# Optimization experiments

Measured on AMD Instinct MI355X. Metric: run time of the kernel, lower is better.

## Reference

```python
import jax, jax.numpy as jnp
import numpy as np

CONV_SPECS = [(1, 64, 4, 2), (64, 128, 8, 4), (128, 256, 10, 5), (256, 256, 12, 6)]  # (cin, cout, k, stride)
N_CODEBOOKS = 8
CODEBOOK_SIZE = 1024
D_MODEL = 256
STATE_FRAMES = 4
B = 8192


def setup_inputs() -> dict:
    key = jax.random.key(0)
    ks = jax.random.split(key, 3 + 2 * len(CONV_SPECS) + 1)
    d = {
        "audio_frame": jax.random.normal(ks[0], (B, 1, 240), dtype=jnp.float32),
        "state_in": jax.random.normal(ks[1], (B, D_MODEL, STATE_FRAMES), dtype=jnp.float32),
    }
    for i, (cin, cout, k, s) in enumerate(CONV_SPECS):
        scale = 1.0 / np.sqrt(cin * k)
        d[f"W{i}"] = jax.random.normal(ks[2 + 2 * i], (cout, cin, k), dtype=jnp.float32) * scale
        d[f"b{i}"] = jnp.zeros((cout,), dtype=jnp.float32)
    d["codebooks"] = jax.random.normal(ks[-1], (N_CODEBOOKS, CODEBOOK_SIZE, D_MODEL), dtype=jnp.float32) * 0.02
    return d


def _causal_conv(x, W, b, stride):
    # x: [B, Cin, L]; causal left-pad of (k - stride) so L_out = L // stride
    k = W.shape[-1]
    x = jnp.pad(x, ((0, 0), (0, 0), (k - stride, 0)))
    y = jax.lax.conv_general_dilated(
        x, W, window_strides=(stride,), padding="VALID",
        dimension_numbers=("NCH", "OIH", "NCH"))
    return y + b[None, :, None]


def _rvq_indices(x_btd, codebooks):
    # x_btd: [B, T, D]; codebooks: [Q, K, D] -> indices [B, Q, T]
    r = x_btd
    idxs = []
    for q in range(codebooks.shape[0]):
        cb = codebooks[q]                                        # [K, D]
        # ||r - c||^2 = ||r||^2 - 2 r.c + ||c||^2 ; ||r||^2 constant over k for argmin
        dist = jnp.sum(cb * cb, axis=-1) - 2.0 * jnp.einsum("btd,kd->btk", r, cb)
        idx = jnp.argmin(dist, axis=-1)                          # [B, T]
        r = r - cb[idx]                                          # residual update
        idxs.append(idx)
    return jnp.stack(idxs, axis=1)                               # [B, Q, T]


def reference(audio_frame, state_in, W0, b0, W1, b1, W2, b2, W3, b3, codebooks):
    # state: roll left, zero last frame
    new_state = jnp.roll(state_in, -1, axis=2).at[:, :, -1].set(0.0)

    # causal conv encoder stack (ELU between conv blocks)
    Ws, bs = (W0, W1, W2, W3), (b0, b1, b2, b3)
    x = audio_frame
    for i, (_, _, _, stride) in enumerate(CONV_SPECS):
        x = _causal_conv(x, Ws[i], bs[i], stride)
        if i < len(CONV_SPECS) - 1:
            x = jax.nn.elu(x)
    # x: [B, D_MODEL, 1]

    new_state = new_state.at[:, :, -1].set(x[:, :, -1])

    z = _rvq_indices(x.transpose(0, 2, 1), codebooks)            # [B, Q, T]
    acoustic_tokens = z[:, :, -1]                                # [B, 8]
    return acoustic_tokens, new_state
```

## Files before the change

kernel.cpp:

```cpp
#include <hip/hip_runtime.h>
#include <hip/hip_bf16.h>

#define GB 2

__device__ __forceinline__ float elu1(float v) { return v > 0.f ? v : expm1f(v); }

__global__ void cnorm_kernel(const float* __restrict__ cb, float* __restrict__ cnorm) {
    int g = blockIdx.x * blockDim.x + threadIdx.x;
    if (g >= 8 * 1024) return;
    const float* p = cb + (size_t)g * 256;
    float s = 0.f;
    for (int d = 0; d < 256; d += 4) {
        float4 v = *reinterpret_cast<const float4*>(p + d);
        s += v.x * v.x + v.y * v.y + v.z * v.z + v.w * v.w;
    }
    cnorm[g] = s;
}

__global__ void cbtrans_kernel(const float* __restrict__ cb, float* __restrict__ cbT) {
    int t = blockIdx.x * blockDim.x + threadIdx.x;
    int o = t * 4;
    const int s = o >> 13;
    const int r = o & 8191;
    const int dl = r >> 10;
    const int k = r & 1023;
    const int q = s >> 5;
    const int d = (s & 31) * 8 + dl;
    const float* src = cb + ((size_t)(q * 1024 + k)) * 256 + d;
    float4 v;
    v.x = src[0 * 256]; v.y = src[1 * 256]; v.z = src[2 * 256]; v.w = src[3 * 256];
    *reinterpret_cast<float4*>(cbT + o) = v;
}

__global__ void wtrans_kernel(const float* __restrict__ W1, const float* __restrict__ W2,
                              const float* __restrict__ W3, float* __restrict__ W1T,
                              float* __restrict__ W2T, float* __restrict__ W3T) {
    int g = blockIdx.x * blockDim.x + threadIdx.x;
    if (g < 8192) {
        int ci = g >> 7, c = g & 127;
        const float* src = W1 + c * 512 + ci * 8;
        float4 a = *reinterpret_cast<const float4*>(src);
        float4 b = *reinterpret_cast<const float4*>(src + 4);
        *reinterpret_cast<float4*>(W1T + g * 8) = a;
        *reinterpret_cast<float4*>(W1T + g * 8 + 4) = b;
    }
    int g2 = g - 8192;
    if (g2 >= 0 && g2 < 32768) {
        int ci = g2 >> 8, c = g2 & 255;
        const float* src = W2 + c * 1280 + ci * 10;
        float* dst = W2T + g2 * 10;
#pragma unroll
        for (int j = 0; j < 5; ++j)
            *reinterpret_cast<float2*>(dst + 2 * j) =
                *reinterpret_cast<const float2*>(src + 2 * j);
    }
    int g3 = g - 40960;
    if (g3 >= 0 && g3 < 65536) {
        int ci = g3 >> 8, c = g3 & 255;
        const float* src = W3 + c * 3072 + ci * 12 + 6;
        float* dst = W3T + g3 * 6;
#pragma unroll
        for (int j = 0; j < 3; ++j)
            *reinterpret_cast<float2*>(dst + 2 * j) =
                *reinterpret_cast<const float2*>(src + 2 * j);
    }
}

__global__ __launch_bounds__(256, 2)
void convA_kernel(const float* __restrict__ audio,
                  const float* __restrict__ W0, const float* __restrict__ b0,
                  const float* __restrict__ W1T, const float* __restrict__ b1,
                  float* __restrict__ y1g) {
    __shared__ __align__(16) float xs[244];
    __shared__ __align__(16) float y0s[64 * 124];

    const int tid = threadIdx.x;
    const int b = blockIdx.x;

    if (tid < 64) {
        y0s[tid * 124 + 0] = 0.f; y0s[tid * 124 + 1] = 0.f;
        y0s[tid * 124 + 2] = 0.f; y0s[tid * 124 + 3] = 0.f;
    }
    if (tid < 242) xs[tid] = (tid < 2) ? 0.f : audio[b * 240 + tid - 2];
    __syncthreads();
    {
        const int ci = tid >> 2, tg = tid & 3;
        float4 w = *reinterpret_cast<const float4*>(W0 + ci * 4);
        float bias = b0[ci];
        for (int t = tg; t < 120; t += 4) {
            float v = bias + w.x * xs[2 * t] + w.y * xs[2 * t + 1]
                           + w.z * xs[2 * t + 2] + w.w * xs[2 * t + 3];
            y0s[ci * 124 + 4 + t] = elu1(v);
        }
    }
    __syncthreads();
    {
        const int c = tid >> 1, half = tid & 1, t0 = 15 * half;
        float acc[15];
        float bias = b1[c];
#pragma unroll
        for (int u = 0; u < 15; ++u) acc[u] = bias;
        const float* wbase = W1T + c * 8;
        const float* ybase = y0s + 4 * t0;
        for (int ci = 0; ci < 64; ++ci) {
            float4 wA = *reinterpret_cast<const float4*>(wbase + ci * 1024);
            float4 wB = *reinterpret_cast<const float4*>(wbase + ci * 1024 + 4);
            const float* yb = ybase + ci * 124;
            float4 row4[16];
#pragma unroll
            for (int j = 0; j < 16; ++j)
                row4[j] = *reinterpret_cast<const float4*>(yb + 4 * j);
#pragma unroll
            for (int u = 0; u < 15; ++u) {
                acc[u] += wA.x * row4[u].x + wA.y * row4[u].y
                        + wA.z * row4[u].z + wA.w * row4[u].w
                        + wB.x * row4[u + 1].x + wB.y * row4[u + 1].y
                        + wB.z * row4[u + 1].z + wB.w * row4[u + 1].w;
            }
        }
        float* yo = y1g + ((size_t)b * 128 + c) * 32 + t0;
#pragma unroll
        for (int u = 0; u < 15; ++u) yo[u] = elu1(acc[u]);
    }
}

__global__ __launch_bounds__(256, 2)
void convB_kernel(const float* __restrict__ state_in,
                  const float* __restrict__ b2, const float* __restrict__ b3,
                  const float* __restrict__ W2T, const float* __restrict__ W3T,
                  const float* __restrict__ y1g,
                  float* __restrict__ out, float* __restrict__ r_ws) {
    __shared__ __align__(16) float y2s[GB * 256 * 6];

    const int tid = threadIdx.x;
    const int bbase = blockIdx.x * GB;

    {
        const int c = tid;
        float acc[GB][6];
        float bias = b2[c];
#pragma unroll
        for (int bi = 0; bi < GB; ++bi)
#pragma unroll
            for (int t = 0; t < 6; ++t) acc[bi][t] = bias;
        const float* wbase = W2T + c * 10;
        for (int ci = 0; ci < 128; ++ci) {
            float w[10];
#pragma unroll
            for (int jj = 0; jj < 5; ++jj) {
                float2 wv = *reinterpret_cast<const float2*>(wbase + ci * 2560 + jj * 2);
                w[jj * 2] = wv.x; w[jj * 2 + 1] = wv.y;
            }
#pragma unroll
            for (int bi = 0; bi < GB; ++bi) {
                const float* yr = y1g + ((size_t)(bbase + bi) * 128 + ci) * 32;
                float row[32];
#pragma unroll
                for (int k4 = 0; k4 < 8; ++k4) {
                    float4 v = *reinterpret_cast<const float4*>(yr + k4 * 4);
                    row[k4 * 4] = v.x; row[k4 * 4 + 1] = v.y;
                    row[k4 * 4 + 2] = v.z; row[k4 * 4 + 3] = v.w;
                }
                acc[bi][0] += w[5] * row[0] + w[6] * row[1] + w[7] * row[2]
                            + w[8] * row[3] + w[9] * row[4];
#pragma unroll
                for (int t = 1; t < 6; ++t) {
                    const int q0 = 5 * t - 5;
                    float s = 0.f;
#pragma unroll
                    for (int j = 0; j < 10; ++j) s += w[j] * row[q0 + j];
                    acc[bi][t] += s;
                }
            }
        }
#pragma unroll
        for (int bi = 0; bi < GB; ++bi)
#pragma unroll
            for (int t = 0; t < 6; ++t)
                y2s[(bi * 256 + c) * 6 + t] = elu1(acc[bi][t]);
    }
    __syncthreads();
    {
        const int c = tid;
        float acc[GB];
        float bias = b3[c];
#pragma unroll
        for (int bi = 0; bi < GB; ++bi) acc[bi] = bias;
        const float* wbase = W3T + c * 6;
        for (int ci = 0; ci < 256; ++ci) {
            float2 w01 = *reinterpret_cast<const float2*>(wbase + ci * 1536);
            float2 w23 = *reinterpret_cast<const float2*>(wbase + ci * 1536 + 2);
            float2 w45 = *reinterpret_cast<const float2*>(wbase + ci * 1536 + 4);
#pragma unroll
            for (int bi = 0; bi < GB; ++bi) {
                const float* yr = y2s + (bi * 256 + ci) * 6;
                float2 a = *reinterpret_cast<const float2*>(yr);
                float2 d = *reinterpret_cast<const float2*>(yr + 2);
                float2 e = *reinterpret_cast<const float2*>(yr + 4);
                acc[bi] += w01.x * a.x + w01.y * a.y + w23.x * d.x + w23.y * d.y
                         + w45.x * e.x + w45.y * e.y;
            }
        }
#pragma unroll
        for (int bi = 0; bi < GB; ++bi) {
            const int b = bbase + bi;
            float y3 = acc[bi];
            r_ws[b * 256 + c] = y3;
            float4 si = *reinterpret_cast<const float4*>(state_in + b * 1024 + c * 4);
            float4 o; o.x = si.y; o.y = si.z; o.z = si.w; o.w = y3;
            *reinterpret_cast<float4*>(out + 65536 + b * 1024 + c * 4) = o;
        }
    }
}

__device__ __forceinline__ unsigned long long distkey(float d, int k) {
    unsigned u = __float_as_uint(d);
    u = (u & 0x80000000u) ? ~u : (u | 0x80000000u);
    return ((unsigned long long)u << 32) | (unsigned)k;
}

__global__ __launch_bounds__(256)
void rvq_kernel(const float* __restrict__ cb, const float* __restrict__ cbT,
                const float* __restrict__ cnorm, const float* __restrict__ r_ws,
                float* __restrict__ out) {
    __shared__ __align__(16) float rs[16 * 256];
    __shared__ unsigned long long part_sh[2][16];
    __shared__ int idx_sh[16];

    const int tid = threadIdx.x;
    const int lane = tid & 63;
    const int wid = tid >> 6;
    const int bg = wid >> 1;
    const int kg = wid & 1;
    const int b0 = blockIdx.x * 16;
    const int kb = kg * 512 + 4 * lane;

    for (int it = 0; it < 4; ++it) {
        int o = (it * 256 + tid) * 4;
        *reinterpret_cast<float4*>(rs + o) =
            *reinterpret_cast<const float4*>(r_ws + b0 * 256 + o);
    }
    __syncthreads();

    for (int q = 0; q < 8; ++q) {
        float acc[8][8];
#pragma unroll
        for (int i = 0; i < 8; ++i)
#pragma unroll
            for (int j = 0; j < 8; ++j) acc[i][j] = 0.f;

        for (int ds = 0; ds < 32; ++ds) {
            const float* sb = cbT + (size_t)(q * 32 + ds) * 8192;
#pragma unroll
            for (int dp = 0; dp < 2; ++dp) {
                float4 cv0[4], cv1[4];
#pragma unroll
                for (int dd = 0; dd < 4; ++dd) {
                    const int dl = dp * 4 + dd;
                    cv0[dd] = *reinterpret_cast<const float4*>(sb + dl * 1024 + kb);
                    cv1[dd] = *reinterpret_cast<const float4*>(sb + dl * 1024 + kb + 256);
                }
                float rr[8][4];
#pragma unroll
                for (int i = 0; i < 8; ++i) {
                    float4 t = *reinterpret_cast<const float4*>(
                        rs + (bg * 8 + i) * 256 + ds * 8 + dp * 4);
                    rr[i][0] = t.x; rr[i][1] = t.y; rr[i][2] = t.z; rr[i][3] = t.w;
                }
#pragma unroll
                for (int dd = 0; dd < 4; ++dd) {
#pragma unroll
                    for (int i = 0; i < 8; ++i) {
                        const float r = rr[i][dd];
                        acc[i][0] += r * cv0[dd].x; acc[i][1] += r * cv0[dd].y;
                        acc[i][2] += r * cv0[dd].z; acc[i][3] += r * cv0[dd].w;
                        acc[i][4] += r * cv1[dd].x; acc[i][5] += r * cv1[dd].y;
                        acc[i][6] += r * cv1[dd].z; acc[i][7] += r * cv1[dd].w;
                    }
                }
            }
        }
        {
            float4 cn0 = *reinterpret_cast<const float4*>(cnorm + q * 1024 + kb);
            float4 cn1 = *reinterpret_cast<const float4*>(cnorm + q * 1024 + kb + 256);
            float c0e[4] = {cn0.x, cn0.y, cn0.z, cn0.w};
            float c1e[4] = {cn1.x, cn1.y, cn1.z, cn1.w};
#pragma unroll
            for (int i = 0; i < 8; ++i) {
                unsigned long long k = 0xFFFFFFFFFFFFFFFFull;
#pragma unroll
                for (int e = 0; e < 4; ++e) {
                    unsigned long long ka = distkey(c0e[e] - 2.f * acc[i][e], kb + e);
                    unsigned long long kc = distkey(c1e[e] - 2.f * acc[i][4 + e],
                                                    kb + 256 + e);
                    if (ka < k) k = ka;
                    if (kc < k) k = kc;
                }
                for (int off = 32; off >= 1; off >>= 1) {
                    unsigned long long o = __shfl_xor(k, off, 64);
                    if (o < k) k = o;
                }
                if (lane == 0) part_sh[kg][bg * 8 + i] = k;
            }
        }
        __syncthreads();
        if (tid < 16) {
            unsigned long long ka = part_sh[0][tid];
            unsigned long long kc = part_sh[1][tid];
            if (kc < ka) ka = kc;
            const int idx = (int)(ka & 0xFFFFFFFFu);
            idx_sh[tid] = idx;
            out[(b0 + tid) * 8 + q] = (float)idx;
        }
        __syncthreads();
        for (int it = 0; it < 16; ++it) {
            const int idx = idx_sh[it];
            rs[it * 256 + tid] -= cb[((size_t)(q * 1024 + idx)) * 256 + tid];
        }
        __syncthreads();
    }
}

extern "C" void kernel_launch(void* const* d_in, const int* in_sizes, int n_in,
                              void* d_out, int out_size, void* d_ws, size_t ws_size,
                              hipStream_t stream) {
    const float* audio = (const float*)d_in[0];
    const float* state = (const float*)d_in[1];
    const float* W0 = (const float*)d_in[2];
    const float* b0 = (const float*)d_in[3];
    const float* W1 = (const float*)d_in[4];
    const float* b1 = (const float*)d_in[5];
    const float* W2 = (const float*)d_in[6];
    const float* b2 = (const float*)d_in[7];
    const float* W3 = (const float*)d_in[8];
    const float* b3 = (const float*)d_in[9];
    const float* cbk = (const float*)d_in[10];
    float* out = (float*)d_out;

    float* cnorm_ws = (float*)d_ws;
    float* r_ws = cnorm_ws + 8192;
    float* W1T = r_ws + 2097152;
    float* W2T = W1T + 65536;
    float* W3T = W2T + 327680;
    float* y1g = W3T + 393216;
    float* cbT = y1g + 33554432;

    cnorm_kernel<<<32, 256, 0, stream>>>(cbk, cnorm_ws);
    cbtrans_kernel<<<2048, 256, 0, stream>>>(cbk, cbT);
    wtrans_kernel<<<416, 256, 0, stream>>>(W1, W2, W3, W1T, W2T, W3T);
    convA_kernel<<<8192, 256, 0, stream>>>(audio, W0, b0, W1T, b1, y1g);
    convB_kernel<<<8192 / GB, 256, 0, stream>>>(state, b2, b3, W2T, W3T, y1g,
                                                out, r_ws);
    rvq_kernel<<<512, 256, 0, stream>>>(cbk, cbT, cnorm_ws, r_ws, out);
}
```

Baseline: 1.868 ms.

## Process two batch items per convA block with two output channels per thread

```diff
diff --git a/kernel.cpp b/kernel.cpp
--- a/kernel.cpp
+++ b/kernel.cpp
@@ -72,39 +72,47 @@
                   const float* __restrict__ W1T, const float* __restrict__ b1,
                   float* __restrict__ y1g) {
     __shared__ __align__(16) float xs[244];
-    __shared__ __align__(16) float y0s[64 * 124];
+    __shared__ __align__(16) float y0s[2 * 64 * 124];
 
     const int tid = threadIdx.x;
-    const int b = blockIdx.x;
-
-    if (tid < 64) {
-        y0s[tid * 124 + 0] = 0.f; y0s[tid * 124 + 1] = 0.f;
-        y0s[tid * 124 + 2] = 0.f; y0s[tid * 124 + 3] = 0.f;
-    }
-    if (tid < 242) xs[tid] = (tid < 2) ? 0.f : audio[b * 240 + tid - 2];
-    __syncthreads();
-    {
+    const int bbase = blockIdx.x * 2;
+
+    if (tid < 128) {
+        const int bz = tid >> 6, ciz = tid & 63;
+        float* p = y0s + (bz * 64 + ciz) * 124;
+        p[0] = 0.f; p[1] = 0.f; p[2] = 0.f; p[3] = 0.f;
+    }
+
+    for (int bi2 = 0; bi2 < 2; ++bi2) {
+        __syncthreads();
+        if (tid < 242) xs[tid] = (tid < 2) ? 0.f : audio[(bbase + bi2) * 240 + tid - 2];
+        __syncthreads();
         const int ci = tid >> 2, tg = tid & 3;
         float4 w = *reinterpret_cast<const float4*>(W0 + ci * 4);
         float bias = b0[ci];
         for (int t = tg; t < 120; t += 4) {
             float v = bias + w.x * xs[2 * t] + w.y * xs[2 * t + 1]
                            + w.z * xs[2 * t + 2] + w.w * xs[2 * t + 3];
-            y0s[ci * 124 + 4 + t] = elu1(v);
+            y0s[(bi2 * 64 + ci) * 124 + 4 + t] = elu1(v);
         }
     }
     __syncthreads();
     {
-        const int c = tid >> 1, half = tid & 1, t0 = 15 * half;
-        float acc[15];
-        float bias = b1[c];
-#pragma unroll
-        for (int u = 0; u < 15; ++u) acc[u] = bias;
-        const float* wbase = W1T + c * 8;
-        const float* ybase = y0s + 4 * t0;
+        const int bi = tid >> 7;
+        const int half = (tid >> 6) & 1;
+        const int cg = tid & 63;
+        const int t0 = 15 * half;
+        float acc0[15], acc1[15];
+        const float bias0 = b1[cg], bias1 = b1[cg + 64];
+#pragma unroll
+        for (int u = 0; u < 15; ++u) { acc0[u] = bias0; acc1[u] = bias1; }
+        const float* wbase0 = W1T + cg * 8;
+        const float* ybase = y0s + bi * 64 * 124 + 4 * t0;
         for (int ci = 0; ci < 64; ++ci) {
-            float4 wA = *reinterpret_cast<const float4*>(wbase + ci * 1024);
-            float4 wB = *reinterpret_cast<const float4*>(wbase + ci * 1024 + 4);
+            float4 wA0 = *reinterpret_cast<const float4*>(wbase0 + ci * 1024);
+            float4 wB0 = *reinterpret_cast<const float4*>(wbase0 + ci * 1024 + 4);
+            float4 wA1 = *reinterpret_cast<const float4*>(wbase0 + ci * 1024 + 512);
+            float4 wB1 = *reinterpret_cast<const float4*>(wbase0 + ci * 1024 + 516);
             const float* yb = ybase + ci * 124;
             float4 row4[16];
 #pragma unroll
@@ -112,15 +120,24 @@
                 row4[j] = *reinterpret_cast<const float4*>(yb + 4 * j);
 #pragma unroll
             for (int u = 0; u < 15; ++u) {
-                acc[u] += wA.x * row4[u].x + wA.y * row4[u].y
-                        + wA.z * row4[u].z + wA.w * row4[u].w
-                        + wB.x * row4[u + 1].x + wB.y * row4[u + 1].y
-                        + wB.z * row4[u + 1].z + wB.w * row4[u + 1].w;
-            }
-        }
-        float* yo = y1g + ((size_t)b * 128 + c) * 32 + t0;
-#pragma unroll
-        for (int u = 0; u < 15; ++u) yo[u] = elu1(acc[u]);
+                acc0[u] += wA0.x * row4[u].x + wA0.y * row4[u].y
+                         + wA0.z * row4[u].z + wA0.w * row4[u].w
+                         + wB0.x * row4[u + 1].x + wB0.y * row4[u + 1].y
+                         + wB0.z * row4[u + 1].z + wB0.w * row4[u + 1].w;
+                acc1[u] += wA1.x * row4[u].x + wA1.y * row4[u].y
+                         + wA1.z * row4[u].z + wA1.w * row4[u].w
+                         + wB1.x * row4[u + 1].x + wB1.y * row4[u + 1].y
+                         + wB1.z * row4[u + 1].z + wB1.w * row4[u + 1].w;
+            }
+        }
+        const int b = bbase + bi;
+        float* yo0 = y1g + ((size_t)b * 128 + cg) * 32 + t0;
+        float* yo1 = y1g + ((size_t)b * 128 + cg + 64) * 32 + t0;
+#pragma unroll
+        for (int u = 0; u < 15; ++u) {
+            yo0[u] = elu1(acc0[u]);
+            yo1[u] = elu1(acc1[u]);
+        }
     }
 }
 
@@ -348,7 +365,7 @@
     cnorm_kernel<<<32, 256, 0, stream>>>(cbk, cnorm_ws);
     cbtrans_kernel<<<2048, 256, 0, stream>>>(cbk, cbT);
     wtrans_kernel<<<416, 256, 0, stream>>>(W1, W2, W3, W1T, W2T, W3T);
-    convA_kernel<<<8192, 256, 0, stream>>>(audio, W0, b0, W1T, b1, y1g);
+    convA_kernel<<<4096, 256, 0, stream>>>(audio, W0, b0, W1T, b1, y1g);
     convB_kernel<<<8192 / GB, 256, 0, stream>>>(state, b2, b3, W2T, W3T, y1g,
                                                 out, r_ws);
     rvq_kernel<<<512, 256, 0, stream>>>(cbk, cbT, cnorm_ws, r_ws, out);
```

Result: faster. 1.789 ms (median of 2 runs) (-4.2%).
